# Kernel tuning notes

Measured on AMD Instinct MI355X. Metric: run time of the kernel, lower is better.

Reference implementation:

```python
import jax, jax.numpy as jnp
import numpy as np

B, D_IN, UNITS = 8192, 4096, 4096

def setup_inputs() -> dict:
    key = jax.random.key(0)
    k1, k2 = jax.random.split(key)
    x = jax.random.normal(k1, (B, D_IN), dtype=jnp.float32)
    kernel = jax.random.normal(k2, (D_IN, UNITS), dtype=jnp.float32) * 0.02  # glorot-ish scale
    bias = jnp.zeros((UNITS,), dtype=jnp.float32)
    return {"x": x, "kernel": kernel, "bias": bias}

def reference(x, kernel, bias):
    # BinaryDense: binarize weights via sign, then dense matmul + bias
    kernel_bin = jnp.sign(kernel)                     # [D_IN, UNITS], values in {-1,0,+1}
    out = jnp.matmul(x, kernel_bin) + bias            # [B, UNITS]
    return out
```

## Files before the change

kernel.cpp:

```cpp
#include <hip/hip_runtime.h>
#include <stdint.h>


typedef int int4v __attribute__((ext_vector_type(4)));

constexpr int M = 8192, N = 4096, K = 4096;
constexpr int BM = 128, BN = 128, BK = 64;

__device__ __forceinline__ void gload_lds16(const void* g, void* l) {
  __builtin_amdgcn_global_load_lds(
      (const __attribute__((address_space(1))) unsigned int*)g,
      (__attribute__((address_space(3))) unsigned int*)l, 16, 0, 0);
}

__global__ __launch_bounds__(256) void quant_x_kernel(const float* __restrict__ x,
                                                      signed char* __restrict__ xq,
                                                      float* __restrict__ rscale) {
  const int row = blockIdx.x;
  const int t = threadIdx.x;
  const float* xr = x + (size_t)row * K;
  float4 v[4];
  float mx = 0.f;
#pragma unroll
  for (int i = 0; i < 4; ++i) {
    v[i] = *(const float4*)(xr + t * 16 + i * 4);
    mx = fmaxf(mx, fmaxf(fmaxf(fabsf(v[i].x), fabsf(v[i].y)),
                         fmaxf(fabsf(v[i].z), fabsf(v[i].w))));
  }
#pragma unroll
  for (int off = 32; off >= 1; off >>= 1)
    mx = fmaxf(mx, __shfl_xor(mx, off, 64));
  __shared__ float smax[4];
  if ((t & 63) == 0) smax[t >> 6] = mx;
  __syncthreads();
  const float rm = fmaxf(fmaxf(smax[0], smax[1]), fmaxf(smax[2], smax[3]));
  const float s = (rm > 0.f) ? 127.f / rm : 0.f;
  if (t == 0) rscale[row] = (rm > 0.f) ? rm / 127.f : 0.f;
  uint32_t o[4];
#pragma unroll
  for (int i = 0; i < 4; ++i) {
    float f[4] = {v[i].x, v[i].y, v[i].z, v[i].w};
    uint32_t p = 0;
#pragma unroll
    for (int j = 0; j < 4; ++j) {
      int q = (int)rintf(f[j] * s);
      p |= ((uint32_t)(uint8_t)(signed char)q) << (8 * j);
    }
    o[i] = p;
  }
  *(int4v*)(xq + (size_t)row * K + t * 16) = (int4v){(int)o[0], (int)o[1], (int)o[2], (int)o[3]};
}

__global__ __launch_bounds__(256) void sign_t_kernel(const float* __restrict__ w,
                                                     signed char* __restrict__ wq) {
  __shared__ __align__(16) signed char tile[64 * 68];
  const int n0 = blockIdx.x * 64, k0 = blockIdx.y * 64;
  const int t = threadIdx.x;
#pragma unroll
  for (int i = 0; i < 4; ++i) {
    int kl = (t >> 4) + i * 16;
    int nl = (t & 15) * 4;
    float4 v = *(const float4*)(w + (size_t)(k0 + kl) * N + n0 + nl);
    uint32_t p = 0;
    p |= ((uint32_t)(uint8_t)(signed char)((v.x > 0.f) - (v.x < 0.f)));
    p |= ((uint32_t)(uint8_t)(signed char)((v.y > 0.f) - (v.y < 0.f))) << 8;
    p |= ((uint32_t)(uint8_t)(signed char)((v.z > 0.f) - (v.z < 0.f))) << 16;
    p |= ((uint32_t)(uint8_t)(signed char)((v.w > 0.f) - (v.w < 0.f))) << 24;
    *(uint32_t*)(tile + kl * 68 + nl) = p;
  }
  __syncthreads();
  const int nl = t >> 2;
  const int kc = (t & 3) * 16;
  uint32_t o[4] = {0, 0, 0, 0};
#pragma unroll
  for (int j = 0; j < 16; ++j)
    o[j >> 2] |= ((uint32_t)(uint8_t)tile[(kc + j) * 68 + nl]) << (8 * (j & 3));
  *(int4v*)(wq + (size_t)(n0 + nl) * K + k0 + kc) =
      (int4v){(int)o[0], (int)o[1], (int)o[2], (int)o[3]};
}

__global__ __launch_bounds__(256) void gemm_bin_kernel(
    const signed char* __restrict__ Xq,
    const signed char* __restrict__ Wq,
    const float* __restrict__ rscale,
    const float* __restrict__ bias,
    float* __restrict__ out) {
  __shared__ __align__(16) signed char Alds[BM * BK];
  __shared__ __align__(16) signed char Blds[BN * BK];

  const int tid = threadIdx.x;
  const int w = tid >> 6;
  const int lane = tid & 63;
  const int wm = w & 1, wn = w >> 1;
  const int m0 = blockIdx.y * BM;
  const int n0 = blockIdx.x * BN;
  const int quad = lane >> 4;
  const int l16 = lane & 15;

  int4v acc[4][4];
#pragma unroll
  for (int i = 0; i < 4; ++i)
#pragma unroll
    for (int j = 0; j < 4; ++j)
      acc[i][j] = (int4v){0, 0, 0, 0};

  for (int k0 = 0; k0 < K; k0 += BK) {
#pragma unroll
    for (int it = 0; it < 2; ++it) {
      int p = it * 256 + tid;
      int row = p >> 2;
      int chunk = (p & 3) ^ ((row >> 1) & 3);
      gload_lds16(Xq + (size_t)(m0 + row) * K + k0 + chunk * 16,
                  Alds + (size_t)(it * 256 + w * 64) * 16);
    }
#pragma unroll
    for (int it = 0; it < 2; ++it) {
      int p = it * 256 + tid;
      int row = p >> 2;
      int chunk = (p & 3) ^ ((row >> 1) & 3);
      gload_lds16(Wq + (size_t)(n0 + row) * K + k0 + chunk * 16,
                  Blds + (size_t)(it * 256 + w * 64) * 16);
    }
    __syncthreads();

    int4v a[4], b[4];
#pragma unroll
    for (int mi = 0; mi < 4; ++mi) {
      int r = wm * 64 + mi * 16 + l16;
      int cpos = (r << 2) | (quad ^ ((r >> 1) & 3));
      a[mi] = *(const int4v*)(Alds + (size_t)cpos * 16);
    }
#pragma unroll
    for (int ni = 0; ni < 4; ++ni) {
      int r = wn * 64 + ni * 16 + l16;
      int cpos = (r << 2) | (quad ^ ((r >> 1) & 3));
      b[ni] = *(const int4v*)(Blds + (size_t)cpos * 16);
    }
#pragma unroll
    for (int mi = 0; mi < 4; ++mi)
#pragma unroll
      for (int ni = 0; ni < 4; ++ni)
        acc[mi][ni] = __builtin_amdgcn_mfma_i32_16x16x64_i8(a[mi], b[ni], acc[mi][ni], 0, 0, 0);

    __syncthreads();
  }

  float sc[4][4];
#pragma unroll
  for (int mi = 0; mi < 4; ++mi) {
    int rbase = m0 + wm * 64 + mi * 16 + quad * 4;
#pragma unroll
    for (int r = 0; r < 4; ++r) sc[mi][r] = rscale[rbase + r];
  }
#pragma unroll
  for (int ni = 0; ni < 4; ++ni) {
    int col = n0 + wn * 64 + ni * 16 + l16;
    float bv = bias[col];
#pragma unroll
    for (int mi = 0; mi < 4; ++mi) {
      int rbase = m0 + wm * 64 + mi * 16 + quad * 4;
#pragma unroll
      for (int r = 0; r < 4; ++r)
        out[(size_t)(rbase + r) * N + col] = (float)acc[mi][ni][r] * sc[mi][r] + bv;
    }
  }
}

extern "C" void kernel_launch(void* const* d_in, const int* in_sizes, int n_in,
                              void* d_out, int out_size, void* d_ws, size_t ws_size,
                              hipStream_t stream) {
  const float* x = (const float*)d_in[0];
  const float* kern = (const float*)d_in[1];
  const float* bias = (const float*)d_in[2];
  float* out = (float*)d_out;

  signed char* Xq = (signed char*)d_ws;
  signed char* Wq = Xq + (size_t)M * K;
  float* rscale = (float*)(Wq + (size_t)N * K);

  quant_x_kernel<<<M, 256, 0, stream>>>(x, Xq, rscale);
  sign_t_kernel<<<dim3(N / 64, K / 64), dim3(256), 0, stream>>>(kern, Wq);
  gemm_bin_kernel<<<dim3(N / BN, M / BM), 256, 0, stream>>>(Xq, Wq, rscale, bias, out);
}
```

Measured before the change: 428.7 us.

## Rewrite int8 GEMM with 256x256 tiles and 8-phase double-buffered LDS pipeline

Raises the GEMM block tile to 256x256x128 with 512 threads and double-buffered 128KB LDS. The main loop is split into eight phases that interleave half-tile global-to-LDS prefetches with MFMA work, using explicit waitcnt, barriers and s_setprio. The aim is to hide load latency behind compute and raise arithmetic intensity per byte loaded, replacing the old single-buffered loop that synchronised every k-step. In exchange, 128KB of LDS allows only one block per CU, the accumulators raise register pressure, and the hand-tuned vmcnt counts are fragile.

```diff
diff --git a/kernel.cpp b/kernel.cpp
--- a/kernel.cpp
+++ b/kernel.cpp
@@ -5,7 +5,9 @@
 typedef int int4v __attribute__((ext_vector_type(4)));
 
 constexpr int M = 8192, N = 4096, K = 4096;
-constexpr int BM = 128, BN = 128, BK = 64;
+constexpr int BM = 256, BN = 256, BK = 128;
+constexpr int NT = K / BK;
+constexpr int NIT = NT / 2;
 
 __device__ __forceinline__ void gload_lds16(const void* g, void* l) {
   __builtin_amdgcn_global_load_lds(
@@ -79,89 +81,133 @@
       (int4v){(int)o[0], (int)o[1], (int)o[2], (int)o[3]};
 }
 
-__global__ __launch_bounds__(256) void gemm_bin_kernel(
+
+#define PHASE(BUF, MIH, NIH, LOADB, ...)                                         \
+  {                                                                              \
+    asm volatile("s_waitcnt vmcnt(6)" ::: "memory");                             \
+    int4v a_[4][2];                                                              \
+    _Pragma("unroll") for (int mi_ = 0; mi_ < 4; ++mi_) {                        \
+      _Pragma("unroll") for (int kk_ = 0; kk_ < 2; ++kk_) {                      \
+        const int row_ = wm * 128 + ((MIH)*4 + mi_) * 16 + l16;                  \
+        const int c_ = kk_ * 4 + quad;                                           \
+        a_[mi_][kk_] = *(const int4v*)(smem + (BUF)*65536 + row_ * 128 +         \
+                                       ((c_ ^ (row_ & 7)) * 16));                \
+      }                                                                          \
+    }                                                                            \
+    if (LOADB) {                                                                 \
+      _Pragma("unroll") for (int nj_ = 0; nj_ < 2; ++nj_) {                      \
+        _Pragma("unroll") for (int kk_ = 0; kk_ < 2; ++kk_) {                    \
+          const int row_ = wn * 64 + ((NIH)*2 + nj_) * 16 + l16;                 \
+          const int c_ = kk_ * 4 + quad;                                         \
+          breg[nj_][kk_] = *(const int4v*)(smem + (BUF)*65536 + 32768 +          \
+                                           row_ * 128 + ((c_ ^ (row_ & 7)) * 16)); \
+        }                                                                        \
+      }                                                                          \
+    }                                                                            \
+    __VA_ARGS__;                                                                 \
+    __builtin_amdgcn_s_barrier();                                                \
+    asm volatile("s_waitcnt lgkmcnt(0)" ::: "memory");                           \
+    __builtin_amdgcn_s_setprio(1);                                               \
+    _Pragma("unroll") for (int mi_ = 0; mi_ < 4; ++mi_) {                        \
+      _Pragma("unroll") for (int nj_ = 0; nj_ < 2; ++nj_) {                      \
+        _Pragma("unroll") for (int kk_ = 0; kk_ < 2; ++kk_) {                    \
+          acc[(MIH)*4 + mi_][(NIH)*2 + nj_] =                                    \
+              __builtin_amdgcn_mfma_i32_16x16x64_i8(                             \
+                  a_[mi_][kk_], breg[nj_][kk_],                                  \
+                  acc[(MIH)*4 + mi_][(NIH)*2 + nj_], 0, 0, 0);                   \
+        }                                                                        \
+      }                                                                          \
+    }                                                                            \
+    __builtin_amdgcn_s_setprio(0);                                               \
+    __builtin_amdgcn_s_barrier();                                                \
+  }
+
+__global__ __launch_bounds__(512, 2) void gemm_bin_kernel(
     const signed char* __restrict__ Xq,
     const signed char* __restrict__ Wq,
     const float* __restrict__ rscale,
     const float* __restrict__ bias,
     float* __restrict__ out) {
-  __shared__ __align__(16) signed char Alds[BM * BK];
-  __shared__ __align__(16) signed char Blds[BN * BK];
+  __shared__ __align__(16) signed char smem[131072];
 
   const int tid = threadIdx.x;
   const int w = tid >> 6;
   const int lane = tid & 63;
-  const int wm = w & 1, wn = w >> 1;
-  const int m0 = blockIdx.y * BM;
-  const int n0 = blockIdx.x * BN;
+  const int wm = w >> 2;
+  const int wn = w & 3;
   const int quad = lane >> 4;
   const int l16 = lane & 15;
-
-  int4v acc[4][4];
-#pragma unroll
-  for (int i = 0; i < 4; ++i)
-#pragma unroll
-    for (int j = 0; j < 4; ++j)
-      acc[i][j] = (int4v){0, 0, 0, 0};
-
-  for (int k0 = 0; k0 < K; k0 += BK) {
+  const size_t m0 = (size_t)blockIdx.y * BM;
+  const size_t n0 = (size_t)blockIdx.x * BN;
+
+  int4v acc[8][4];
+#pragma unroll
+  for (int i = 0; i < 8; ++i)
+#pragma unroll
+    for (int j = 0; j < 4; ++j) acc[i][j] = (int4v){0, 0, 0, 0};
+  int4v breg[2][2];
+
+  auto stageA = [&](int buf, int half, int tile) {
+    signed char* lb = smem + buf * 65536;
 #pragma unroll
     for (int it = 0; it < 2; ++it) {
-      int p = it * 256 + tid;
-      int row = p >> 2;
-      int chunk = (p & 3) ^ ((row >> 1) & 3);
-      gload_lds16(Xq + (size_t)(m0 + row) * K + k0 + chunk * 16,
-                  Alds + (size_t)(it * 256 + w * 64) * 16);
-    }
+      int pos = it * 512 + tid;
+      int rr = pos >> 3, s = pos & 7;
+      int row = half * 64 + (rr & 63) + (rr >> 6) * 128;
+      int qg = s ^ (row & 7);
+      gload_lds16(Xq + (m0 + row) * (size_t)K + (size_t)tile * BK + qg * 16,
+                  lb + row * 128 + s * 16);
+    }
+  };
+  auto stageB = [&](int buf, int half, int tile) {
+    signed char* lb = smem + buf * 65536 + 32768;
 #pragma unroll
     for (int it = 0; it < 2; ++it) {
-      int p = it * 256 + tid;
-      int row = p >> 2;
-      int chunk = (p & 3) ^ ((row >> 1) & 3);
-      gload_lds16(Wq + (size_t)(n0 + row) * K + k0 + chunk * 16,
-                  Blds + (size_t)(it * 256 + w * 64) * 16);
-    }
-    __syncthreads();
-
-    int4v a[4], b[4];
-#pragma unroll
-    for (int mi = 0; mi < 4; ++mi) {
-      int r = wm * 64 + mi * 16 + l16;
-      int cpos = (r << 2) | (quad ^ ((r >> 1) & 3));
-      a[mi] = *(const int4v*)(Alds + (size_t)cpos * 16);
-    }
+      int pos = it * 512 + tid;
+      int rr = pos >> 3, s = pos & 7;
+      int row = half * 32 + (rr & 31) + (rr >> 5) * 64;
+      int qg = s ^ (row & 7);
+      gload_lds16(Wq + (n0 + row) * (size_t)K + (size_t)tile * BK + qg * 16,
+                  lb + row * 128 + s * 16);
+    }
+  };
+
+  stageB(0, 0, 0);
+  stageA(0, 0, 0);
+  stageA(0, 1, 0);
+  stageB(0, 1, 0);
+  stageB(1, 0, 1);
+  stageA(1, 0, 1);
+  asm volatile("s_waitcnt vmcnt(6)" ::: "memory");
+  __builtin_amdgcn_s_barrier();
+
+#pragma unroll 1
+  for (int i = 0; i < NIT; ++i) {
+    const int t1 = 2 * i + 1, t2 = 2 * i + 2, t3 = 2 * i + 3;
+    const bool more = (i + 1 < NIT);
+    PHASE(0, 0, 0, true,  { stageA(1, 1, t1); })
+    PHASE(0, 1, 0, false, { stageB(1, 1, t1); })
+    PHASE(0, 0, 1, true,  { if (more) stageB(0, 0, t2); })
+    PHASE(0, 1, 1, false, { if (more) stageA(0, 0, t2); })
+    PHASE(1, 0, 0, true,  { if (more) stageA(0, 1, t2); })
+    PHASE(1, 1, 0, false, { if (more) stageB(0, 1, t2); })
+    PHASE(1, 0, 1, true,  { if (more) stageB(1, 0, t3); })
+    PHASE(1, 1, 1, false, { if (more) stageA(1, 0, t3); })
+  }
+
+#pragma unroll
+  for (int mi = 0; mi < 8; ++mi) {
+    const size_t rbase = m0 + wm * 128 + mi * 16 + quad * 4;
+    float sc[4];
+#pragma unroll
+    for (int r = 0; r < 4; ++r) sc[r] = rscale[rbase + r];
 #pragma unroll
     for (int ni = 0; ni < 4; ++ni) {
-      int r = wn * 64 + ni * 16 + l16;
-      int cpos = (r << 2) | (quad ^ ((r >> 1) & 3));
-      b[ni] = *(const int4v*)(Blds + (size_t)cpos * 16);
-    }
-#pragma unroll
-    for (int mi = 0; mi < 4; ++mi)
-#pragma unroll
-      for (int ni = 0; ni < 4; ++ni)
-        acc[mi][ni] = __builtin_amdgcn_mfma_i32_16x16x64_i8(a[mi], b[ni], acc[mi][ni], 0, 0, 0);
-
-    __syncthreads();
-  }
-
-  float sc[4][4];
-#pragma unroll
-  for (int mi = 0; mi < 4; ++mi) {
-    int rbase = m0 + wm * 64 + mi * 16 + quad * 4;
-#pragma unroll
-    for (int r = 0; r < 4; ++r) sc[mi][r] = rscale[rbase + r];
-  }
-#pragma unroll
-  for (int ni = 0; ni < 4; ++ni) {
-    int col = n0 + wn * 64 + ni * 16 + l16;
-    float bv = bias[col];
-#pragma unroll
-    for (int mi = 0; mi < 4; ++mi) {
-      int rbase = m0 + wm * 64 + mi * 16 + quad * 4;
+      const size_t col = n0 + wn * 64 + ni * 16 + l16;
+      const float bv = bias[col];
 #pragma unroll
       for (int r = 0; r < 4; ++r)
-        out[(size_t)(rbase + r) * N + col] = (float)acc[mi][ni][r] * sc[mi][r] + bv;
+        out[(rbase + r) * N + col] = (float)acc[mi][ni][r] * sc[r] + bv;
     }
   }
 }
@@ -180,5 +226,5 @@
 
   quant_x_kernel<<<M, 256, 0, stream>>>(x, Xq, rscale);
   sign_t_kernel<<<dim3(N / 64, K / 64), dim3(256), 0, stream>>>(kern, Wq);
-  gemm_bin_kernel<<<dim3(N / BN, M / BM), 256, 0, stream>>>(Xq, Wq, rscale, bias, out);
-}
+  gemm_bin_kernel<<<dim3(N / BN, M / BM), 512, 0, stream>>>(Xq, Wq, rscale, bias, out);
+}
```

Measured after the change: 394.6 us. -8.0%, faster.
